# Kernel optimization log

Measured on AMD Instinct MI355X. Metric: run time of the kernel, lower is better.

Reference implementation:

```python
import jax, jax.numpy as jnp
import numpy as np
import math

B, S, DIM, HEADS = 2, 2048, 1024, 16


def _alibi_slopes(n_heads):
    def pow2_slopes(n):
        start = 2 ** (-2 ** (-(math.log2(n) - 3)))
        return [start * start ** i for i in range(n)]
    if math.log2(n_heads).is_integer():
        slopes = pow2_slopes(n_heads)
    else:
        closest = 2 ** math.floor(math.log2(n_heads))
        slopes = pow2_slopes(closest)
        slopes += pow2_slopes(2 * closest)[0::2][: n_heads - closest]
    return np.asarray(slopes, dtype=np.float32).reshape(n_heads, 1, 1)


def setup_inputs() -> dict:
    key = jax.random.key(0)
    k1, k2, k3 = jax.random.split(key, 3)
    x = jax.random.normal(k1, (B, S, DIM), dtype=jnp.float32)
    W_qkv = jax.random.normal(k2, (3 * DIM, DIM), dtype=jnp.float32) * 0.02
    W_o = jax.random.normal(k3, (DIM, DIM), dtype=jnp.float32) * 0.02
    return {"x": x, "W_qkv": W_qkv, "W_o": W_o}


def reference(x, W_qkv, W_o):
    b, s, d = x.shape
    h = HEADS
    hd = d // h
    scale = hd ** -0.5

    qkv = x @ W_qkv.T                                   # (b, s, 3d)
    q, k, v = jnp.split(qkv, 3, axis=-1)
    q = q.reshape(b, s, h, hd).transpose(0, 2, 1, 3)    # (b, h, s, hd)
    k = k.reshape(b, s, h, hd).transpose(0, 2, 1, 3)
    v = v.reshape(b, s, h, hd).transpose(0, 2, 1, 3)

    scores = jnp.einsum('bhqd,bhkd->bhqk', q, k) * scale  # (b, h, s, s)

    pos = jnp.arange(s)
    rel = (pos[None, :] - pos[:, None]).astype(scores.dtype)  # j - i, (s, s)
    slopes = jnp.asarray(_alibi_slopes(h))                     # (h, 1, 1)
    scores = scores - slopes * rel                             # broadcast over (b,)

    causal_mask = pos[None, :] > pos[:, None]                  # True above diag
    scores = jnp.where(causal_mask, jnp.finfo(scores.dtype).min, scores)

    weights = jax.nn.softmax(scores, axis=-1)
    out = jnp.einsum('bhqk,bhkd->bhqd', weights, v)            # (b, h, s, hd)
    out = out.transpose(0, 2, 1, 3).reshape(b, s, d)
    return out @ W_o.T
```

## Files before the change

kernel.cpp:

```cpp
#include <hip/hip_runtime.h>

typedef unsigned short u16;
typedef unsigned int u32;
typedef __attribute__((ext_vector_type(8))) __bf16 bf16x8;
typedef __attribute__((ext_vector_type(4))) float f32x4;
typedef __attribute__((ext_vector_type(4))) u32 u32x4;


static __device__ __forceinline__ u16 f2bf(float f) {
  unsigned u = __builtin_bit_cast(unsigned, f);
  u += 0x7FFFu + ((u >> 16) & 1u);
  return (u16)(u >> 16);
}
static __device__ __forceinline__ float bf2f(u16 v) {
  return __builtin_bit_cast(float, (u32)v << 16);
}

static __device__ __forceinline__ void gload_lds16(const void* g, void* l) {
  __builtin_amdgcn_global_load_lds(
      (const __attribute__((address_space(1))) unsigned int*)g,
      (__attribute__((address_space(3))) unsigned int*)l, 16, 0, 0);
}

__global__ __launch_bounds__(256) void cvt_all(const float* __restrict__ x,
                                               const float* __restrict__ wq,
                                               const float* __restrict__ wo,
                                               u16* __restrict__ xb,
                                               u16* __restrict__ wqb,
                                               u16* __restrict__ wob) {
  int i = blockIdx.x * 256 + threadIdx.x;
  const float* src;
  u16* dst;
  int off;
  if (i < 1048576) {
    src = x; dst = xb; off = i;
  } else if (i < 1048576 + 786432) {
    src = wq; dst = wqb; off = i - 1048576;
  } else {
    src = wo; dst = wob; off = i - 1835008;
  }
  float4 f = ((const float4*)src)[off];
  uint2 o;
  o.x = (unsigned)f2bf(f.x) | ((unsigned)f2bf(f.y) << 16);
  o.y = (unsigned)f2bf(f.z) | ((unsigned)f2bf(f.w) << 16);
  ((uint2*)dst)[off] = o;
}

__global__ __launch_bounds__(256, 2) void gemm_qkv(
    const u16* __restrict__ A, const u16* __restrict__ Bm, int K,
    u16* __restrict__ qo, u16* __restrict__ ko, u16* __restrict__ vo) {
  __shared__ __align__(16) u16 SH[2][128 * 64];
  const int tid = threadIdx.x;
  const int lane = tid & 63, w = tid >> 6;
  const int wr = w >> 1, wc = w & 1;
  const int hfl = blockIdx.y * gridDim.x + blockIdx.x;
  const int qq = (gridDim.x * gridDim.y) >> 3;
  const int wid = (hfl & 7) * qq + (hfl >> 3);
  const int m0 = (wid % gridDim.y) * 128;
  const int n0 = (wid / gridDim.y) * 128;
  const int c16 = lane >> 4, r16 = lane & 15;

  const f32x4 zero4 = {0.f, 0.f, 0.f, 0.f};
  f32x4 acc[4][4];
#pragma unroll
  for (int r = 0; r < 4; ++r)
#pragma unroll
    for (int c = 0; c < 4; ++c) acc[r][c] = zero4;

  const int nk = K >> 6;

  auto stage = [&](int kt) {
#pragma unroll
    for (int i = 0; i < 4; ++i) {
      const int chunk = w * 4 + i;
      const int lb = chunk * 1024 + lane * 16;
      const int row = lb >> 7;
      const int rb = (lb & 127) ^ ((row & 7) << 4);
      gload_lds16(A + (size_t)(m0 + row) * K + kt * 64 + (rb >> 1),
                  (char*)&SH[0][0] + chunk * 1024);
      gload_lds16(Bm + (size_t)(n0 + row) * K + kt * 64 + (rb >> 1),
                  (char*)&SH[1][0] + chunk * 1024);
    }
  };

  stage(0);
  __syncthreads();
  for (int kt = 0; kt < nk; ++kt) {
#pragma unroll
    for (int ks = 0; ks < 2; ++ks) {
      bf16x8 af[4], bfv[4];
#pragma unroll
      for (int r = 0; r < 4; ++r) {
        const int ra = wr * 64 + r * 16 + r16;
        af[r] = *(const bf16x8*)((const char*)&SH[0][0] +
                ((ra * 128 + ks * 64 + c16 * 16) ^ ((ra & 7) << 4)));
        const int rbn = wc * 64 + r * 16 + r16;
        bfv[r] = *(const bf16x8*)((const char*)&SH[1][0] +
                ((rbn * 128 + ks * 64 + c16 * 16) ^ ((rbn & 7) << 4)));
      }
#pragma unroll
      for (int r = 0; r < 4; ++r)
#pragma unroll
        for (int c = 0; c < 4; ++c)
          acc[r][c] = __builtin_amdgcn_mfma_f32_16x16x32_bf16(
              af[r], bfv[c], acc[r][c], 0, 0, 0);
    }
    __syncthreads();
    if (kt + 1 < nk) stage(kt + 1);
    __syncthreads();
  }

  if (n0 < 2048) {
    const float qs = (n0 < 1024) ? 0.18033688f : 1.0f;
    u16* dst0 = (n0 < 1024) ? qo : ko;
#pragma unroll
    for (int r = 0; r < 4; ++r)
#pragma unroll
      for (int c = 0; c < 4; ++c)
#pragma unroll
        for (int b = 0; b < 4; ++b) {
          const int row = m0 + wr * 64 + r * 16 + 4 * c16 + b;
          const int col = n0 + wc * 64 + c * 16 + r16;
          const int hh = (col & 1023) >> 6, hd = col & 63;
          const int bi = row >> 11, s = row & 2047;
          dst0[((size_t)(bi * 16 + hh) * 2048 + s) * 64 + hd] =
              f2bf(acc[r][c][b] * qs);
        }
  } else {
#pragma unroll
    for (int r = 0; r < 4; ++r)
#pragma unroll
      for (int c = 0; c < 4; ++c)
#pragma unroll
        for (int b = 0; b < 4; b += 2) {
          const int row_l = wr * 64 + r * 16 + 4 * c16 + b;
          const int col_l = wc * 64 + c * 16 + r16;
          const u32 val = (u32)f2bf(acc[r][c][b]) |
                          ((u32)f2bf(acc[r][c][b + 1]) << 16);
          *(u32*)((char*)&SH[0][0] +
                  ((col_l * 256 + (row_l >> 1) * 4) ^ ((col_l & 7) << 4))) = val;
        }
    __syncthreads();
    const int col_l = tid >> 1, half = tid & 1;
    const int hh = (n0 - 2048 + col_l) >> 6, hd = (n0 - 2048 + col_l) & 63;
    const int bi = m0 >> 11;
    u16* dst = vo + ((size_t)(bi * 16 + hh) * 64 + hd) * 2048 +
               (m0 & 2047) + half * 64;
#pragma unroll
    for (int j = 0; j < 8; ++j) {
      const uint4 v4 = *(const uint4*)((const char*)&SH[0][0] +
          (col_l * 256 + ((half * 128 + j * 16) ^ ((col_l & 7) << 4))));
      *(uint4*)(dst + j * 8) = v4;
    }
  }
}

__global__ __launch_bounds__(128, 3) void gemm_proj(
    const u16* __restrict__ A, const u16* __restrict__ Bm, int K, int N,
    float* __restrict__ fo) {
  __shared__ __align__(16) u16 Asm[64 * 64];
  __shared__ __align__(16) u16 Bsm[128 * 64];
  const int tid = threadIdx.x;
  const int lane = tid & 63, w = tid >> 6;
  const int hfl = blockIdx.y * gridDim.x + blockIdx.x;
  const int qq = (gridDim.x * gridDim.y) >> 3;
  const int wid = (hfl & 7) * qq + (hfl >> 3);
  const int m0 = (wid % gridDim.y) * 64;
  const int n0 = (wid / gridDim.y) * 128;
  const int c16 = lane >> 4, r16 = lane & 15;

  const f32x4 zero4 = {0.f, 0.f, 0.f, 0.f};
  f32x4 acc[4][4];
#pragma unroll
  for (int r = 0; r < 4; ++r)
#pragma unroll
    for (int c = 0; c < 4; ++c) acc[r][c] = zero4;

  const int nk = K >> 6;

  auto stage = [&](int kt) {
#pragma unroll
    for (int i = 0; i < 4; ++i) {
      const int chunk = w * 4 + i;
      const int lb = chunk * 1024 + lane * 16;
      const int row = lb >> 7;
      const int rb = (lb & 127) ^ ((row & 7) << 4);
      gload_lds16(A + (size_t)(m0 + row) * K + kt * 64 + (rb >> 1),
                  (char*)&Asm[0] + chunk * 1024);
    }
#pragma unroll
    for (int i = 0; i < 8; ++i) {
      const int chunk = w * 8 + i;
      const int lb = chunk * 1024 + lane * 16;
      const int row = lb >> 7;
      const int rb = (lb & 127) ^ ((row & 7) << 4);
      gload_lds16(Bm + (size_t)(n0 + row) * K + kt * 64 + (rb >> 1),
                  (char*)&Bsm[0] + chunk * 1024);
    }
  };

  stage(0);
  __syncthreads();
  for (int kt = 0; kt < nk; ++kt) {
#pragma unroll
    for (int ks = 0; ks < 2; ++ks) {
      bf16x8 af[4], bfv[4];
#pragma unroll
      for (int r = 0; r < 4; ++r) {
        const int ra = r * 16 + r16;
        af[r] = *(const bf16x8*)((const char*)&Asm[0] +
                ((ra * 128 + ks * 64 + c16 * 16) ^ ((ra & 7) << 4)));
        const int rbn = w * 64 + r * 16 + r16;
        bfv[r] = *(const bf16x8*)((const char*)&Bsm[0] +
                ((rbn * 128 + ks * 64 + c16 * 16) ^ ((rbn & 7) << 4)));
      }
#pragma unroll
      for (int r = 0; r < 4; ++r)
#pragma unroll
        for (int c = 0; c < 4; ++c)
          acc[r][c] = __builtin_amdgcn_mfma_f32_16x16x32_bf16(
              af[r], bfv[c], acc[r][c], 0, 0, 0);
    }
    __syncthreads();
    if (kt + 1 < nk) stage(kt + 1);
    __syncthreads();
  }

#pragma unroll
  for (int r = 0; r < 4; ++r)
#pragma unroll
    for (int c = 0; c < 4; ++c)
#pragma unroll
      for (int b = 0; b < 4; ++b) {
        const int row = m0 + r * 16 + 4 * c16 + b;
        const int col = n0 + w * 64 + c * 16 + r16;
        fo[(size_t)row * N + col] = acc[r][c][b];
      }
}

__global__ __launch_bounds__(256, 5) void attn_part(const u16* __restrict__ qb,
                                                    const u16* __restrict__ kb,
                                                    const u16* __restrict__ vtb,
                                                    u16* __restrict__ ob,
                                                    u16* __restrict__ Op,
                                                    float* __restrict__ ml) {
  __shared__ __align__(16) u16 Kl[2][64 * 64];
  __shared__ __align__(16) u16 Vt[2][64 * 64];

  const int tid = threadIdx.x;
  const int lane = tid & 63, w = tid >> 6;
  const int lo = lane & 15, hi = lane >> 4;
  const int yb = blockIdx.y;
  const int h = 15 - (yb >> 1), bi = yb & 1;
  const int bh = bi * 16 + h;
  const int y = blockIdx.x;

  int qt, t0, t1, slot = 0;
  bool part;
  if (y < 16) {
    qt = 31 - y;
    const int T = qt + 1;
    t0 = T >> 1; t1 = T; part = true;
    slot = bh * 32 + (qt - 16) * 2 + 1;
  } else if (y < 32) {
    qt = 47 - y;
    const int T = qt + 1;
    t0 = 0; t1 = T >> 1; part = true;
    slot = bh * 32 + (qt - 16) * 2;
  } else {
    qt = 47 - y;
    t0 = 0; t1 = qt + 1; part = false;
  }

  const int q0 = qt * 64;
  const float slope2 = exp2f(-0.5f * (float)(h + 1)) * 1.44269504089f;
  const float s64 = slope2 * 64.f;

  const int Dt = min(32, (int)ceilf(34.f / s64));
  t1 = min(t1, Dt);

  if (part && t0 >= t1) {
#pragma unroll
    for (int g = 0; g < 4; ++g)
#pragma unroll
      for (int r = 0; r < 4; ++r) {
        const int sl = w * 16 + 4 * hi + r;
        Op[(size_t)slot * 4096 + sl * 64 + g * 16 + lo] = 0;
      }
    if (hi == 0) ml[slot * 64 + w * 16 + lo] = 0.f;
    return;
  }

  const u16* __restrict__ Q = qb + (size_t)bh * 131072;
  const u16* __restrict__ Kp = kb + (size_t)bh * 131072;
  const u16* __restrict__ Vp = vtb + (size_t)bh * 131072;

  auto stageK = [&](int t, int buf) {
#pragma unroll
    for (int i = 0; i < 2; ++i) {
      const int chunk = w * 2 + i;
      const int lb = chunk * 1024 + lane * 16;
      const int row = lb >> 7;
      const int rb = (lb & 127) ^ ((row & 7) << 4);
      gload_lds16(Kp + (size_t)(t * 64 + row) * 64 + (rb >> 1),
                  (char*)&Kl[buf][0] + chunk * 1024);
    }
  };
  auto stageV = [&](int t, int buf) {
#pragma unroll
    for (int i = 0; i < 2; ++i) {
      const int chunk = w * 2 + i;
      const int lb = chunk * 1024 + lane * 16;
      const int row = lb >> 7;
      const int rb = (lb & 127) ^ ((row & 7) << 4);
      gload_lds16(Vp + (size_t)row * 2048 + t * 64 + (rb >> 1),
                  (char*)&Vt[buf][0] + chunk * 1024);
    }
  };

  bf16x8 qf[2];
  {
    const u16* qsrc = Q + (size_t)(q0 + w * 16 + lo) * 64 + hi * 8;
    qf[0] = *(const bf16x8*)qsrc;
    qf[1] = *(const bf16x8*)(qsrc + 32);
  }

  const f32x4 zero4 = {0.f, 0.f, 0.f, 0.f};
  f32x4 oacc[4];
#pragma unroll
  for (int g = 0; g < 4; ++g) oacc[g] = zero4;
  float lsum = 0.f;

  float KC[4][4];
#pragma unroll
  for (int g = 0; g < 4; ++g)
#pragma unroll
    for (int r = 0; r < 4; ++r)
      KC[g][r] = slope2 * (float)(16 * g + 4 * hi + r);
  float ctv = 0.f;

  stageK(t0, 0);
  stageV(t0, 0);
  __syncthreads();

  for (int t = t0; t < t1; ++t) {
    const int cur = (t - t0) & 1, nxt = cur ^ 1;
    if (t + 1 < t1) {
      stageK(t + 1, nxt);
      stageV(t + 1, nxt);
    }

    f32x4 st[4];
#pragma unroll
    for (int g = 0; g < 4; ++g) {
#pragma unroll
      for (int r = 0; r < 4; ++r) st[g][r] = ctv - KC[g][r];
#pragma unroll
      for (int ks = 0; ks < 2; ++ks) {
        const int krow = g * 16 + lo;
        const bf16x8 kf = *(const bf16x8*)((const char*)&Kl[cur][0] +
            ((krow * 128 + ks * 64 + hi * 16) ^ ((krow & 7) << 4)));
        st[g] = __builtin_amdgcn_mfma_f32_16x16x32_bf16(kf, qf[ks], st[g], 0, 0, 0);
      }
    }

    if (t == qt) {
#pragma unroll
      for (int g = 0; g < 4; ++g)
#pragma unroll
        for (int r = 0; r < 4; ++r)
          if (g * 16 + 4 * hi + r > w * 16 + lo) st[g][r] = -1e30f;
    }
    float p[4][4];
    float rs = 0.f;
#pragma unroll
    for (int g = 0; g < 4; ++g)
#pragma unroll
      for (int r = 0; r < 4; ++r) {
        p[g][r] = exp2f(st[g][r]);
        rs += p[g][r];
      }
    lsum += rs;

    u32 pk[4][2];
#pragma unroll
    for (int g = 0; g < 4; ++g)
#pragma unroll
      for (int c = 0; c < 2; ++c)
        pk[g][c] = __builtin_amdgcn_perm(
            __builtin_bit_cast(u32, p[g][2 * c + 1]),
            __builtin_bit_cast(u32, p[g][2 * c]), 0x07060302u);

    bf16x8 pA[2];
#pragma unroll
    for (int u = 0; u < 2; ++u) {
      const u32 a0 = pk[2 * u][0], a1 = pk[2 * u][1];
      const u32 b0 = pk[2 * u + 1][0], b1 = pk[2 * u + 1][1];
      const u32 s10 = __shfl_xor((hi & 2) ? a0 : b0, 32, 64);
      const u32 s11 = __shfl_xor((hi & 2) ? a1 : b1, 32, 64);
      const u32 c0 = (hi & 2) ? s10 : a0, c1 = (hi & 2) ? s11 : a1;
      const u32 d0 = (hi & 2) ? b0 : s10, d1 = (hi & 2) ? b1 : s11;
      const u32 f0 = __shfl_xor((hi & 1) ? c0 : d0, 16, 64);
      const u32 f1 = __shfl_xor((hi & 1) ? c1 : d1, 16, 64);
      u32x4 wv;
      wv.x = (hi & 1) ? f0 : c0;
      wv.y = (hi & 1) ? f1 : c1;
      wv.z = (hi & 1) ? d0 : f0;
      wv.w = (hi & 1) ? d1 : f1;
      pA[u] = __builtin_bit_cast(bf16x8, wv);
    }

#pragma unroll
    for (int g = 0; g < 4; ++g) {
#pragma unroll
      for (int u = 0; u < 2; ++u) {
        const int vrow = g * 16 + lo;
        const bf16x8 vf = *(const bf16x8*)((const char*)&Vt[cur][0] +
            ((vrow * 128 + u * 64 + hi * 16) ^ ((vrow & 7) << 4)));
        oacc[g] = __builtin_amdgcn_mfma_f32_16x16x32_bf16(pA[u], vf, oacc[g], 0, 0, 0);
      }
    }

    ctv -= s64;
    __syncthreads();
  }

  lsum += __shfl_xor(lsum, 16, 64);
  lsum += __shfl_xor(lsum, 32, 64);
  const float inv = 1.f / lsum;
  float iv[4];
#pragma unroll
  for (int r = 0; r < 4; ++r) iv[r] = __shfl(inv, 4 * hi + r, 64);

  if (!part) {
#pragma unroll
    for (int g = 0; g < 4; ++g)
#pragma unroll
      for (int r = 0; r < 4; ++r) {
        const int s = q0 + w * 16 + 4 * hi + r;
        const int hd = g * 16 + lo;
        ob[(((size_t)bi * 2048 + s) * 16 + h) * 64 + hd] =
            f2bf(oacc[g][r] * iv[r]);
      }
  } else {
#pragma unroll
    for (int g = 0; g < 4; ++g)
#pragma unroll
      for (int r = 0; r < 4; ++r) {
        const int sl = w * 16 + 4 * hi + r;
        Op[(size_t)slot * 4096 + sl * 64 + g * 16 + lo] =
            f2bf(oacc[g][r] * iv[r]);
      }
    if (hi == 0) ml[slot * 64 + w * 16 + lo] = lsum;
  }
}

__global__ __launch_bounds__(256) void attn_comb(const u16* __restrict__ Op,
                                                 const float* __restrict__ ml,
                                                 u16* __restrict__ ob) {
  const int bh = blockIdx.x, q16 = blockIdx.y;
  const int h = bh & 15, bi = bh >> 4;
  const int qt = 16 + q16;
  const int t0c = (qt + 1) >> 1;
  const float slope2 = exp2f(-0.5f * (float)(h + 1)) * 1.44269504089f;
  const float e1 = exp2f(-slope2 * 64.f * (float)t0c);
  const int slot0 = bh * 32 + q16 * 2;
  const int row = threadIdx.x >> 2, c0 = (threadIdx.x & 3) * 16;
  const float l0 = ml[slot0 * 64 + row];
  const float l1 = ml[(slot0 + 1) * 64 + row];
  const float w0 = l0, w1 = l1 * e1;
  const float inv = 1.f / (w0 + w1);
  const float a0 = w0 * inv, a1 = w1 * inv;
  const u16* p0 = Op + (size_t)slot0 * 4096 + row * 64 + c0;
  const u16* p1 = p0 + 4096;
  u32 A0[8], A1[8];
  *(uint4*)&A0[0] = *(const uint4*)p0;
  *(uint4*)&A0[4] = *(const uint4*)(p0 + 8);
  *(uint4*)&A1[0] = *(const uint4*)p1;
  *(uint4*)&A1[4] = *(const uint4*)(p1 + 8);
  const int s = qt * 64 + row;
  u32* dst = (u32*)(ob + (((size_t)bi * 2048 + s) * 16 + h) * 64 + c0);
#pragma unroll
  for (int j = 0; j < 8; ++j) {
    const float e0 = a0 * bf2f((u16)(A0[j] & 0xffffu)) +
                     a1 * bf2f((u16)(A1[j] & 0xffffu));
    const float ee1 = a0 * bf2f((u16)(A0[j] >> 16)) +
                      a1 * bf2f((u16)(A1[j] >> 16));
    dst[j] = (u32)f2bf(e0) | ((u32)f2bf(ee1) << 16);
  }
}

extern "C" void kernel_launch(void* const* d_in, const int* in_sizes, int n_in,
                              void* d_out, int out_size, void* d_ws, size_t ws_size,
                              hipStream_t stream) {
  const float* x = (const float*)d_in[0];
  const float* Wqkv = (const float*)d_in[1];
  const float* Wo = (const float*)d_in[2];
  float* out = (float*)d_out;

  u16* xb  = (u16*)d_ws;
  u16* wqb = xb + 4194304;
  u16* wob = wqb + 3145728;
  u16* qbf = wob + 1048576;
  u16* kbf = qbf + 4194304;
  u16* vbf = kbf + 4194304;
  u16* abf = vbf + 4194304;

  u16* Op = xb;
  float* ml = (float*)wqb;

  cvt_all<<<8192, 256, 0, stream>>>(x, Wqkv, Wo, xb, wqb, wob);

  gemm_qkv<<<dim3(24, 32), 256, 0, stream>>>(xb, wqb, 1024, qbf, kbf, vbf);
  attn_part<<<dim3(48, 32), 256, 0, stream>>>(qbf, kbf, vbf, abf, Op, ml);
  attn_comb<<<dim3(32, 16), 256, 0, stream>>>(Op, ml, abf);
  gemm_proj<<<dim3(8, 64), 128, 0, stream>>>(abf, wob, 1024, 1024, out);
}
```

Measured before the change: 103.8 us.

## Rewrite QKV GEMM as 256x256 tile, 8-wave, double-buffered phased pipeline

Result: slower. 111.8 us (+7.7%).

```diff
diff --git a/kernel.cpp b/kernel.cpp
--- a/kernel.cpp
+++ b/kernel.cpp
@@ -46,110 +46,166 @@
   ((uint2*)dst)[off] = o;
 }
 
-__global__ __launch_bounds__(256, 2) void gemm_qkv(
+
+#define QKV_PHASE(BUF, MH, NH, LDA, LDB, ST, SB, SHH, VM)                     \
+  do {                                                                        \
+    if (LDA) {                                                                \
+      _Pragma("unroll") for (int mf = 0; mf < 4; ++mf) {                      \
+        const int ra = wr * 128 + (MH) * 64 + mf * 16 + r16;                  \
+        const int rx = (ra & 7) << 4;                                         \
+        af[mf][0] = *(const bf16x8*)((const char*)&SH[(BUF) * 2][0] +         \
+                                     ((ra * 128 + c16 * 16) ^ rx));           \
+        af[mf][1] = *(const bf16x8*)((const char*)&SH[(BUF) * 2][0] +         \
+                                     ((ra * 128 + 64 + c16 * 16) ^ rx));      \
+      }                                                                       \
+    }                                                                         \
+    if (LDB) {                                                                \
+      _Pragma("unroll") for (int nf = 0; nf < 2; ++nf) {                      \
+        const int rb = wn * 64 + (NH) * 32 + nf * 16 + r16;                   \
+        const int rx = (rb & 7) << 4;                                         \
+        bfv[nf][0] = *(const bf16x8*)((const char*)&SH[(BUF) * 2 + 1][0] +    \
+                                      ((rb * 128 + c16 * 16) ^ rx));          \
+        bfv[nf][1] = *(const bf16x8*)((const char*)&SH[(BUF) * 2 + 1][0] +    \
+                                      ((rb * 128 + 64 + c16 * 16) ^ rx));     \
+      }                                                                       \
+    }                                                                         \
+    stageHalf((ST), (SB), (SHH));                                             \
+    __builtin_amdgcn_s_barrier();                                             \
+    asm volatile("s_waitcnt lgkmcnt(0)" ::: "memory");                        \
+    __builtin_amdgcn_sched_barrier(0);                                        \
+    __builtin_amdgcn_s_setprio(1);                                            \
+    _Pragma("unroll") for (int mf = 0; mf < 4; ++mf)                          \
+      _Pragma("unroll") for (int nf = 0; nf < 2; ++nf) {                      \
+        acc[(MH) * 4 + mf][(NH) * 2 + nf] =                                   \
+            __builtin_amdgcn_mfma_f32_16x16x32_bf16(                          \
+                af[mf][0], bfv[nf][0], acc[(MH) * 4 + mf][(NH) * 2 + nf],     \
+                0, 0, 0);                                                     \
+        acc[(MH) * 4 + mf][(NH) * 2 + nf] =                                   \
+            __builtin_amdgcn_mfma_f32_16x16x32_bf16(                          \
+                af[mf][1], bfv[nf][1], acc[(MH) * 4 + mf][(NH) * 2 + nf],     \
+                0, 0, 0);                                                     \
+      }                                                                       \
+    __builtin_amdgcn_s_setprio(0);                                            \
+    if ((VM) == 1) {                                                          \
+      if (t + 2 < nk)                                                         \
+        asm volatile("s_waitcnt vmcnt(4)" ::: "memory");                      \
+      else                                                                    \
+        asm volatile("s_waitcnt vmcnt(0)" ::: "memory");                      \
+    }                                                                         \
+    if ((VM) == 2) {                                                          \
+      if (t + 3 < nk)                                                         \
+        asm volatile("s_waitcnt vmcnt(4)" ::: "memory");                      \
+      else                                                                    \
+        asm volatile("s_waitcnt vmcnt(0)" ::: "memory");                      \
+    }                                                                         \
+    __builtin_amdgcn_s_barrier();                                             \
+  } while (0)
+
+__global__ __launch_bounds__(512, 2) void gemm_qkv(
     const u16* __restrict__ A, const u16* __restrict__ Bm, int K,
     u16* __restrict__ qo, u16* __restrict__ ko, u16* __restrict__ vo) {
-  __shared__ __align__(16) u16 SH[2][128 * 64];
+  __shared__ __align__(16) u16 SH[4][16384];
   const int tid = threadIdx.x;
   const int lane = tid & 63, w = tid >> 6;
-  const int wr = w >> 1, wc = w & 1;
+  const int wr = w >> 2, wn = w & 3;
   const int hfl = blockIdx.y * gridDim.x + blockIdx.x;
   const int qq = (gridDim.x * gridDim.y) >> 3;
   const int wid = (hfl & 7) * qq + (hfl >> 3);
-  const int m0 = (wid % gridDim.y) * 128;
-  const int n0 = (wid / gridDim.y) * 128;
+  const int m0 = (wid % gridDim.y) * 256;
+  const int n0 = (wid / gridDim.y) * 256;
   const int c16 = lane >> 4, r16 = lane & 15;
+  const int nk = K >> 6;
 
   const f32x4 zero4 = {0.f, 0.f, 0.f, 0.f};
-  f32x4 acc[4][4];
-#pragma unroll
-  for (int r = 0; r < 4; ++r)
+  f32x4 acc[8][4];
+#pragma unroll
+  for (int r = 0; r < 8; ++r)
 #pragma unroll
     for (int c = 0; c < 4; ++c) acc[r][c] = zero4;
 
-  const int nk = K >> 6;
-
-  auto stage = [&](int kt) {
-#pragma unroll
-    for (int i = 0; i < 4; ++i) {
-      const int chunk = w * 4 + i;
+  const u16* __restrict__ Abase = A + (size_t)m0 * K;
+  const u16* __restrict__ Bbase = Bm + (size_t)n0 * K;
+
+  auto stageHalf = [&](int tile, int isB, int h) {
+    if (tile >= nk) return;
+    const u16* src = isB ? Bbase : Abase;
+    char* dst = (char*)&SH[((tile & 1) << 1) + isB][0] + h * 16384;
+#pragma unroll
+    for (int j = 0; j < 2; ++j) {
+      const int chunk = w * 2 + j;
       const int lb = chunk * 1024 + lane * 16;
-      const int row = lb >> 7;
+      const int row = h * 128 + (lb >> 7);
       const int rb = (lb & 127) ^ ((row & 7) << 4);
-      gload_lds16(A + (size_t)(m0 + row) * K + kt * 64 + (rb >> 1),
-                  (char*)&SH[0][0] + chunk * 1024);
-      gload_lds16(Bm + (size_t)(n0 + row) * K + kt * 64 + (rb >> 1),
-                  (char*)&SH[1][0] + chunk * 1024);
+      gload_lds16(src + (size_t)row * K + tile * 64 + (rb >> 1),
+                  dst + chunk * 1024);
     }
   };
 
-  stage(0);
-  __syncthreads();
-  for (int kt = 0; kt < nk; ++kt) {
-#pragma unroll
-    for (int ks = 0; ks < 2; ++ks) {
-      bf16x8 af[4], bfv[4];
-#pragma unroll
-      for (int r = 0; r < 4; ++r) {
-        const int ra = wr * 64 + r * 16 + r16;
-        af[r] = *(const bf16x8*)((const char*)&SH[0][0] +
-                ((ra * 128 + ks * 64 + c16 * 16) ^ ((ra & 7) << 4)));
-        const int rbn = wc * 64 + r * 16 + r16;
-        bfv[r] = *(const bf16x8*)((const char*)&SH[1][0] +
-                ((rbn * 128 + ks * 64 + c16 * 16) ^ ((rbn & 7) << 4)));
-      }
-#pragma unroll
-      for (int r = 0; r < 4; ++r)
-#pragma unroll
-        for (int c = 0; c < 4; ++c)
-          acc[r][c] = __builtin_amdgcn_mfma_f32_16x16x32_bf16(
-              af[r], bfv[c], acc[r][c], 0, 0, 0);
-    }
-    __syncthreads();
-    if (kt + 1 < nk) stage(kt + 1);
-    __syncthreads();
+  bf16x8 af[4][2], bfv[2][2];
+
+  stageHalf(0, 0, 0);
+  stageHalf(0, 1, 0);
+  stageHalf(0, 0, 1);
+  stageHalf(0, 1, 1);
+  stageHalf(1, 1, 0);
+  stageHalf(1, 0, 1);
+  asm volatile("s_waitcnt vmcnt(4)" ::: "memory");
+  __builtin_amdgcn_s_barrier();
+
+#pragma unroll 1
+  for (int it = 0; it < (nk >> 1); ++it) {
+    const int t = it * 2;
+    QKV_PHASE(0, 0, 0, true, true, t + 1, 1, 1, 0);
+    QKV_PHASE(0, 1, 0, true, false, t + 1, 0, 0, 0);
+    QKV_PHASE(0, 1, 1, false, true, t + 2, 1, 0, 0);
+    QKV_PHASE(0, 0, 1, true, false, t + 2, 0, 1, 1);
+    QKV_PHASE(1, 0, 0, true, true, t + 2, 1, 1, 0);
+    QKV_PHASE(1, 1, 0, true, false, t + 2, 0, 0, 0);
+    QKV_PHASE(1, 1, 1, false, true, t + 3, 1, 0, 0);
+    QKV_PHASE(1, 0, 1, true, false, t + 3, 0, 1, 2);
   }
 
   if (n0 < 2048) {
     const float qs = (n0 < 1024) ? 0.18033688f : 1.0f;
     u16* dst0 = (n0 < 1024) ? qo : ko;
 #pragma unroll
-    for (int r = 0; r < 4; ++r)
-#pragma unroll
-      for (int c = 0; c < 4; ++c)
+    for (int am = 0; am < 8; ++am)
+#pragma unroll
+      for (int an = 0; an < 4; ++an)
 #pragma unroll
         for (int b = 0; b < 4; ++b) {
-          const int row = m0 + wr * 64 + r * 16 + 4 * c16 + b;
-          const int col = n0 + wc * 64 + c * 16 + r16;
+          const int row = m0 + wr * 128 + am * 16 + 4 * c16 + b;
+          const int col = n0 + wn * 64 + an * 16 + r16;
           const int hh = (col & 1023) >> 6, hd = col & 63;
           const int bi = row >> 11, s = row & 2047;
           dst0[((size_t)(bi * 16 + hh) * 2048 + s) * 64 + hd] =
-              f2bf(acc[r][c][b] * qs);
+              f2bf(acc[am][an][b] * qs);
         }
   } else {
 #pragma unroll
-    for (int r = 0; r < 4; ++r)
-#pragma unroll
-      for (int c = 0; c < 4; ++c)
+    for (int am = 0; am < 8; ++am)
+#pragma unroll
+      for (int an = 0; an < 4; ++an)
 #pragma unroll
         for (int b = 0; b < 4; b += 2) {
-          const int row_l = wr * 64 + r * 16 + 4 * c16 + b;
-          const int col_l = wc * 64 + c * 16 + r16;
-          const u32 val = (u32)f2bf(acc[r][c][b]) |
-                          ((u32)f2bf(acc[r][c][b + 1]) << 16);
+          const int s_l = wr * 128 + am * 16 + 4 * c16 + b;
+          const int vcl = wn * 64 + an * 16 + r16;
+          const u32 val = (u32)f2bf(acc[am][an][b]) |
+                          ((u32)f2bf(acc[am][an][b + 1]) << 16);
           *(u32*)((char*)&SH[0][0] +
-                  ((col_l * 256 + (row_l >> 1) * 4) ^ ((col_l & 7) << 4))) = val;
+                  ((vcl * 512 + (s_l >> 1) * 4) ^ ((vcl & 7) << 4))) = val;
         }
     __syncthreads();
-    const int col_l = tid >> 1, half = tid & 1;
-    const int hh = (n0 - 2048 + col_l) >> 6, hd = (n0 - 2048 + col_l) & 63;
+    const int vcl = tid >> 1, half = tid & 1;
+    const int gc = n0 - 2048 + vcl;
+    const int hh = gc >> 6, hd = gc & 63;
     const int bi = m0 >> 11;
-    u16* dst = vo + ((size_t)(bi * 16 + hh) * 64 + hd) * 2048 +
-               (m0 & 2047) + half * 64;
-#pragma unroll
-    for (int j = 0; j < 8; ++j) {
+    u16* dst = vo + ((size_t)(bi * 16 + hh) * 64 + hd) * 2048 + (m0 & 2047) +
+               half * 128;
+#pragma unroll
+    for (int j = 0; j < 16; ++j) {
       const uint4 v4 = *(const uint4*)((const char*)&SH[0][0] +
-          (col_l * 256 + ((half * 128 + j * 16) ^ ((col_l & 7) << 4))));
+          (vcl * 512 + ((half * 256 + j * 16) ^ ((vcl & 7) << 4))));
       *(uint4*)(dst + j * 8) = v4;
     }
   }
@@ -511,7 +567,7 @@
 
   cvt_all<<<8192, 256, 0, stream>>>(x, Wqkv, Wo, xb, wqb, wob);
 
-  gemm_qkv<<<dim3(24, 32), 256, 0, stream>>>(xb, wqb, 1024, qbf, kbf, vbf);
+  gemm_qkv<<<dim3(12, 16), 512, 0, stream>>>(xb, wqb, 1024, qbf, kbf, vbf);
   attn_part<<<dim3(48, 32), 256, 0, stream>>>(qbf, kbf, vbf, abf, Op, ml);
   attn_comb<<<dim3(32, 16), 256, 0, stream>>>(Op, ml, abf);
   gemm_proj<<<dim3(8, 64), 128, 0, stream>>>(abf, wob, 1024, 1024, out);
```

## Fuse split-KV combine into attention kernel via last-arriver atomic counter

Applied to the files above, without the earlier changes.

Measured after the change: 291.3 us. +180.8%, slower.

```diff
diff --git a/kernel.cpp b/kernel.cpp
--- a/kernel.cpp
+++ b/kernel.cpp
@@ -27,8 +27,10 @@
                                                const float* __restrict__ wo,
                                                u16* __restrict__ xb,
                                                u16* __restrict__ wqb,
-                                               u16* __restrict__ wob) {
+                                               u16* __restrict__ wob,
+                                               u32* __restrict__ cnt) {
   int i = blockIdx.x * 256 + threadIdx.x;
+  if (blockIdx.x < 2) cnt[i] = 0;
   const float* src;
   u16* dst;
   int off;
@@ -243,9 +245,11 @@
                                                     const u16* __restrict__ vtb,
                                                     u16* __restrict__ ob,
                                                     u16* __restrict__ Op,
-                                                    float* __restrict__ ml) {
+                                                    float* __restrict__ ml,
+                                                    u32* __restrict__ cnt) {
   __shared__ __align__(16) u16 Kl[2][64 * 64];
   __shared__ __align__(16) u16 Vt[2][64 * 64];
+  __shared__ int who;
 
   const int tid = threadIdx.x;
   const int lane = tid & 63, w = tid >> 6;
@@ -279,6 +283,42 @@
   const int Dt = min(32, (int)ceilf(34.f / s64));
   t1 = min(t1, Dt);
 
+  auto mergeTail = [&]() {
+    __threadfence();
+    __syncthreads();
+    if (tid == 0) who = atomicAdd(&cnt[bh * 16 + (qt - 16)], 1);
+    __syncthreads();
+    if (who == 1) {
+      __threadfence();
+      const int t0c = (qt + 1) >> 1;
+      const float e1 = exp2f(-s64 * (float)t0c);
+      const int slot0 = bh * 32 + (qt - 16) * 2;
+      const int row = tid >> 2, c0 = (tid & 3) * 16;
+      const float l0 = ml[slot0 * 64 + row];
+      const float l1 = ml[(slot0 + 1) * 64 + row];
+      const float w0 = l0, w1 = l1 * e1;
+      const float invw = 1.f / (w0 + w1);
+      const float a0 = w0 * invw, a1 = w1 * invw;
+      const u16* p0 = Op + (size_t)slot0 * 4096 + row * 64 + c0;
+      const u16* p1 = p0 + 4096;
+      u32 A0[8], A1[8];
+      *(uint4*)&A0[0] = *(const uint4*)p0;
+      *(uint4*)&A0[4] = *(const uint4*)(p0 + 8);
+      *(uint4*)&A1[0] = *(const uint4*)p1;
+      *(uint4*)&A1[4] = *(const uint4*)(p1 + 8);
+      const int s = qt * 64 + row;
+      u32* dst = (u32*)(ob + (((size_t)bi * 2048 + s) * 16 + h) * 64 + c0);
+#pragma unroll
+      for (int j = 0; j < 8; ++j) {
+        const float e0 = a0 * bf2f((u16)(A0[j] & 0xffffu)) +
+                         a1 * bf2f((u16)(A1[j] & 0xffffu));
+        const float ee1 = a0 * bf2f((u16)(A0[j] >> 16)) +
+                          a1 * bf2f((u16)(A1[j] >> 16));
+        dst[j] = (u32)f2bf(e0) | ((u32)f2bf(ee1) << 16);
+      }
+    }
+  };
+
   if (part && t0 >= t1) {
 #pragma unroll
     for (int g = 0; g < 4; ++g)
@@ -288,6 +328,7 @@
         Op[(size_t)slot * 4096 + sl * 64 + g * 16 + lo] = 0;
       }
     if (hi == 0) ml[slot * 64 + w * 16 + lo] = 0.f;
+    mergeTail();
     return;
   }
 
@@ -452,41 +493,7 @@
             f2bf(oacc[g][r] * iv[r]);
       }
     if (hi == 0) ml[slot * 64 + w * 16 + lo] = lsum;
-  }
-}
-
-__global__ __launch_bounds__(256) void attn_comb(const u16* __restrict__ Op,
-                                                 const float* __restrict__ ml,
-                                                 u16* __restrict__ ob) {
-  const int bh = blockIdx.x, q16 = blockIdx.y;
-  const int h = bh & 15, bi = bh >> 4;
-  const int qt = 16 + q16;
-  const int t0c = (qt + 1) >> 1;
-  const float slope2 = exp2f(-0.5f * (float)(h + 1)) * 1.44269504089f;
-  const float e1 = exp2f(-slope2 * 64.f * (float)t0c);
-  const int slot0 = bh * 32 + q16 * 2;
-  const int row = threadIdx.x >> 2, c0 = (threadIdx.x & 3) * 16;
-  const float l0 = ml[slot0 * 64 + row];
-  const float l1 = ml[(slot0 + 1) * 64 + row];
-  const float w0 = l0, w1 = l1 * e1;
-  const float inv = 1.f / (w0 + w1);
-  const float a0 = w0 * inv, a1 = w1 * inv;
-  const u16* p0 = Op + (size_t)slot0 * 4096 + row * 64 + c0;
-  const u16* p1 = p0 + 4096;
-  u32 A0[8], A1[8];
-  *(uint4*)&A0[0] = *(const uint4*)p0;
-  *(uint4*)&A0[4] = *(const uint4*)(p0 + 8);
-  *(uint4*)&A1[0] = *(const uint4*)p1;
-  *(uint4*)&A1[4] = *(const uint4*)(p1 + 8);
-  const int s = qt * 64 + row;
-  u32* dst = (u32*)(ob + (((size_t)bi * 2048 + s) * 16 + h) * 64 + c0);
-#pragma unroll
-  for (int j = 0; j < 8; ++j) {
-    const float e0 = a0 * bf2f((u16)(A0[j] & 0xffffu)) +
-                     a1 * bf2f((u16)(A1[j] & 0xffffu));
-    const float ee1 = a0 * bf2f((u16)(A0[j] >> 16)) +
-                      a1 * bf2f((u16)(A1[j] >> 16));
-    dst[j] = (u32)f2bf(e0) | ((u32)f2bf(ee1) << 16);
+    mergeTail();
   }
 }
 
@@ -505,14 +512,14 @@
   u16* kbf = qbf + 4194304;
   u16* vbf = kbf + 4194304;
   u16* abf = vbf + 4194304;
+  u32* cnt = (u32*)(abf + 4194304);
 
   u16* Op = xb;
   float* ml = (float*)wqb;
 
-  cvt_all<<<8192, 256, 0, stream>>>(x, Wqkv, Wo, xb, wqb, wob);
+  cvt_all<<<8192, 256, 0, stream>>>(x, Wqkv, Wo, xb, wqb, wob, cnt);
 
   gemm_qkv<<<dim3(24, 32), 256, 0, stream>>>(xb, wqb, 1024, qbf, kbf, vbf);
-  attn_part<<<dim3(48, 32), 256, 0, stream>>>(qbf, kbf, vbf, abf, Op, ml);
-  attn_comb<<<dim3(32, 16), 256, 0, stream>>>(Op, ml, abf);
+  attn_part<<<dim3(48, 32), 256, 0, stream>>>(qbf, kbf, vbf, abf, Op, ml, cnt);
   gemm_proj<<<dim3(8, 64), 128, 0, stream>>>(abf, wob, 1024, 1024, out);
 }
```
